# Performance work log

Hardware: AMD Instinct MI355X
Metric: run time of the kernel (lower is better)

## Reference

```python
import jax, jax.numpy as jnp
import numpy as np

EMBED_DIM = 1024
NUM_HEADS = 16
HEAD_DIM = EMBED_DIM // NUM_HEADS
SCALE_BASE = EMBED_DIM  # XPOS(head_dim, embed_dim): embed_dim is scale_base
BSZ, SEQ = 8, 1024


def xpos_apply(x, downscale):
    # x: [B*H, L, D]; standard xpos (torchscale) rotary with position-dependent scale
    L, D = x.shape[1], x.shape[2]
    half = D // 2
    s = (jnp.arange(0, D, 2, dtype=jnp.float32) + 0.4 * D) / (1.4 * D)  # [half]
    min_pos = -(L // 2)  # offset = 0
    pos = jnp.arange(min_pos, min_pos + L, dtype=jnp.float32)  # [L]
    scale = s[None, :] ** (pos[:, None] / SCALE_BASE)  # [L, half]
    inv_freq = 1.0 / (10000.0 ** (jnp.arange(half, dtype=jnp.float32) / half))
    sinus = jnp.arange(L, dtype=jnp.float32)[:, None] * inv_freq[None, :]  # [L, half]
    sin, cos = jnp.sin(sinus), jnp.cos(sinus)
    if downscale:
        scale = 1.0 / scale
    # duplicate_interleave: repeat each column twice -> [L, D]
    sin_d = jnp.repeat(sin * scale, 2, axis=-1)
    cos_d = jnp.repeat(cos * scale, 2, axis=-1)
    x1, x2 = x[..., 0::2], x[..., 1::2]
    rot = jnp.stack([-x2, x1], axis=-1).reshape(x.shape)  # rotate_every_two
    return x * cos_d + rot * sin_d


def setup_inputs() -> dict:
    key = jax.random.key(0)
    ks = jax.random.split(key, 12)
    std = 0.02
    inp = {
        'query': jax.random.normal(ks[0], (BSZ, SEQ, EMBED_DIM), jnp.float32),
        'key': jax.random.normal(ks[1], (BSZ, SEQ, EMBED_DIM), jnp.float32),
        'value': jax.random.normal(ks[2], (BSZ, SEQ, EMBED_DIM), jnp.float32),
        'wq': jax.random.normal(ks[3], (EMBED_DIM, EMBED_DIM), jnp.float32) * std,
        'bq': jax.random.normal(ks[4], (EMBED_DIM,), jnp.float32) * std,
        'wk': jax.random.normal(ks[5], (EMBED_DIM, EMBED_DIM), jnp.float32) * std,
        'bk': jax.random.normal(ks[6], (EMBED_DIM,), jnp.float32) * std,
        'wv': jax.random.normal(ks[7], (EMBED_DIM, EMBED_DIM), jnp.float32) * std,
        'bv': jax.random.normal(ks[8], (EMBED_DIM,), jnp.float32) * std,
        'wo': jax.random.normal(ks[9], (EMBED_DIM, EMBED_DIM), jnp.float32) * std,
        'bo': jax.random.normal(ks[10], (EMBED_DIM,), jnp.float32) * std,
    }
    return inp


def reference(query, key, value, wq, bq, wk, bk, wv, bv, wo, bo):
    B, T, E = query.shape
    S = key.shape[1]
    scaling = HEAD_DIM ** -0.5
    q = (query @ wq.T + bq) * scaling
    k = key @ wk.T + bk
    v = value @ wv.T + bv

    def split_heads(x, L):
        return x.reshape(B, L, NUM_HEADS, HEAD_DIM).transpose(0, 2, 1, 3).reshape(B * NUM_HEADS, L, HEAD_DIM)

    q = split_heads(q, T)
    k = split_heads(k, S)
    v = split_heads(v, S)
    k = xpos_apply(k, downscale=True)
    q = xpos_apply(q, downscale=False)
    attn_w = jnp.einsum('btd,bsd->bts', q, k)  # [B*H, T, S]
    attn_w = jax.nn.softmax(attn_w.astype(jnp.float32), axis=-1).astype(q.dtype)
    attn = jnp.einsum('bts,bsd->btd', attn_w, v)  # [B*H, T, D]
    attn = attn.reshape(B, NUM_HEADS, T, HEAD_DIM).transpose(0, 2, 1, 3).reshape(B, T, E)
    return attn @ wo.T + bo
```

## Files before the change

kernel.cpp:

```cpp
#include <hip/hip_runtime.h>


#define BSZ  8
#define SEQ  1024
#define EMB  1024
#define NH   16
#define HD   64
#define HALF 32
#define BH   (BSZ*NH)
#define MROWS (BSZ*SEQ)

typedef __attribute__((ext_vector_type(4))) float f32x4;
typedef __attribute__((ext_vector_type(8))) short bf16x8;

__device__ __forceinline__ ushort f2bf(float f) {
    union { float f; unsigned u; } v; v.f = f;
    return (ushort)((v.u + 0x7FFFu + ((v.u >> 16) & 1u)) >> 16);
}

__device__ __forceinline__ unsigned cvt_pk_bf16(float a, float b) {
    unsigned r;
    asm("v_cvt_pk_bf16_f32 %0, %1, %2" : "=v"(r) : "v"(a), "v"(b));
    return r;
}

__device__ __forceinline__ void async16(void* lds, const void* g) {
    __builtin_amdgcn_global_load_lds(
        (const __attribute__((address_space(1))) unsigned int*)g,
        (__attribute__((address_space(3))) unsigned int*)lds, 16, 0, 0);
}

__global__ __launch_bounds__(256)
void castw_kernel(const float* __restrict__ w0, const float* __restrict__ w1,
                  const float* __restrict__ w2, const float* __restrict__ w3,
                  ushort* __restrict__ d0, ushort* __restrict__ d1,
                  ushort* __restrict__ d2, ushort* __restrict__ d3, int n4) {
    int i = blockIdx.x * 256 + threadIdx.x;
    if (i >= n4) return;
    const float* s = blockIdx.y == 0 ? w0 : blockIdx.y == 1 ? w1
                   : blockIdx.y == 2 ? w2 : w3;
    ushort* d = blockIdx.y == 0 ? d0 : blockIdx.y == 1 ? d1
              : blockIdx.y == 2 ? d2 : d3;
    float4 v = reinterpret_cast<const float4*>(s)[i];
    ushort4 o;
    o.x = f2bf(v.x); o.y = f2bf(v.y); o.z = f2bf(v.z); o.w = f2bf(v.w);
    reinterpret_cast<ushort4*>(d)[i] = o;
}

__global__ __launch_bounds__(256)
void xpos_tables_kernel(float* __restrict__ tab) {
    int idx = blockIdx.x * 256 + threadIdx.x;
    if (idx >= SEQ * HALF) return;
    int t = idx >> 5;
    int j = idx & 31;
    float s        = (2.0f * (float)j + 0.4f * (float)HD) / (1.4f * (float)HD);
    float pos      = (float)(t - SEQ / 2);
    float scale    = powf(s, pos * (1.0f / 1024.0f));
    float inv_freq = powf(10000.0f, -(float)j / (float)HALF);
    float ang      = (float)t * inv_freq;
    float sn = sinf(ang), cs = cosf(ang);
    float inv_scale = 1.0f / scale;
    tab[0 * SEQ * HALF + idx] = sn * scale;
    tab[1 * SEQ * HALF + idx] = cs * scale;
    tab[2 * SEQ * HALF + idx] = sn * inv_scale;
    tab[3 * SEQ * HALF + idx] = cs * inv_scale;
}

__global__ __launch_bounds__(256, 3)
void qkv_gemm_kernel(const float* __restrict__ Aq, const float* __restrict__ Ak,
                     const float* __restrict__ Av,
                     const ushort* __restrict__ Wq, const ushort* __restrict__ Wk,
                     const ushort* __restrict__ Wv,
                     const float* __restrict__ bq, const float* __restrict__ bk,
                     const float* __restrict__ bv,
                     const float* __restrict__ tab,
                     ushort* __restrict__ oq, ushort* __restrict__ ok,
                     ushort* __restrict__ ov) {
    __shared__ float  Asf[128 * 64];
    __shared__ ushort Bs[128 * 64];
    const int ymode = blockIdx.y;
    const float*  A    = ymode == 0 ? Aq : ymode == 1 ? Ak : Av;
    const ushort* W    = ymode == 0 ? Wq : ymode == 1 ? Wk : Wv;
    const float*  bias = ymode == 0 ? bq : ymode == 1 ? bk : bv;
    ushort*       outp = ymode == 0 ? oq : ymode == 1 ? ok : ov;

    const int tid  = threadIdx.x;
    const int lane = tid & 63;
    const int w    = tid >> 6;
    const int g    = lane >> 4;
    const int c    = lane & 15;
    const int wr   = w >> 1, wc = w & 1;

    int lid = blockIdx.x;
    int wg  = (lid & 7) * 64 + (lid >> 3);
    const int row0 = (wg >> 3) * 128;
    const int col0 = (wg & 7) * 128;

    f32x4 acc[4][4] = {};

    int arow[8], acol[8];
    #pragma unroll
    for (int i = 0; i < 8; ++i) {
        int f = i * 4096 + tid * 16;
        int r = f >> 8, pb = f & 255;
        arow[i] = r;
        acol[i] = (pb ^ ((r & 7) << 5)) >> 2;
    }
    int brow[4], bcol[4];
    #pragma unroll
    for (int i = 0; i < 4; ++i) {
        int f = i * 4096 + tid * 16;
        int r = f >> 7, cb = f & 127;
        brow[i] = r;
        bcol[i] = (cb ^ ((r & 7) << 4)) >> 1;
    }

    for (int t = 0; t < 16; ++t) {
        const int k0 = t * 64;
        #pragma unroll
        for (int i = 0; i < 8; ++i)
            async16(&Asf[i * 1024 + w * 256],
                    &A[(size_t)(row0 + arow[i]) * EMB + k0 + acol[i]]);
        #pragma unroll
        for (int i = 0; i < 4; ++i)
            async16(&Bs[i * 2048 + w * 512],
                    &W[(size_t)(col0 + brow[i]) * EMB + k0 + bcol[i]]);
        __syncthreads();

        #pragma unroll
        for (int ks = 0; ks < 2; ++ks) {
            bf16x8 af[4], bfr[4];
            #pragma unroll
            for (int mi = 0; mi < 4; ++mi) {
                int r  = wr * 64 + mi * 16 + c;
                int pb = (ks * 128 + g * 32) ^ ((r & 7) << 5);
                const char* ab = reinterpret_cast<const char*>(Asf) + r * 256 + pb;
                f32x4 a0 = *reinterpret_cast<const f32x4*>(ab);
                f32x4 a1 = *reinterpret_cast<const f32x4*>(ab + 16);
                union { uint4 u; bf16x8 v; } pk;
                pk.u.x = cvt_pk_bf16(a0[0], a0[1]);
                pk.u.y = cvt_pk_bf16(a0[2], a0[3]);
                pk.u.z = cvt_pk_bf16(a1[0], a1[1]);
                pk.u.w = cvt_pk_bf16(a1[2], a1[3]);
                af[mi] = pk.v;
            }
            #pragma unroll
            for (int ni = 0; ni < 4; ++ni) {
                int r = wc * 64 + ni * 16 + c;
                bfr[ni] = *reinterpret_cast<const bf16x8*>(
                    reinterpret_cast<const char*>(Bs) + r * 128 +
                    ((ks * 64 + g * 16) ^ ((r & 7) << 4)));
            }
            #pragma unroll
            for (int mi = 0; mi < 4; ++mi)
                #pragma unroll
                for (int ni = 0; ni < 4; ++ni)
                    acc[mi][ni] = __builtin_amdgcn_mfma_f32_16x16x32_bf16(
                        af[mi], bfr[ni], acc[mi][ni], 0, 0, 0);
        }
        __syncthreads();
    }

    #pragma unroll
    for (int ni = 0; ni < 4; ++ni) {
        int n = col0 + wc * 64 + ni * 16 + c;
        float bn = bias[n];
        #pragma unroll
        for (int mi = 0; mi < 4; ++mi) {
            #pragma unroll
            for (int r = 0; r < 4; ++r) {
                int m = row0 + wr * 64 + mi * 16 + g * 4 + r;
                float val = acc[mi][ni][r] + bn;
                if (ymode == 0) val *= 0.125f;
                if (ymode != 2) {
                    int t2 = m & (SEQ - 1);
                    int d  = n & 63;
                    const int base = (ymode == 0 ? 0 : 2) * SEQ * HALF + t2 * HALF;
                    float sn = tab[base + (d >> 1)];
                    float cs = tab[base + SEQ * HALF + (d >> 1)];
                    float other = __shfl_xor(val, 1);
                    val = val * cs + ((d & 1) ? other * sn : -other * sn);
                }
                int b = m >> 10, t3 = m & 1023;
                int h = n >> 6,  d2 = n & 63;
                outp[(((size_t)b * NH + h) * SEQ + t3) * HD + d2] = f2bf(val);
            }
        }
    }
}

template <int MODE>
__global__ __launch_bounds__(256)
void gemm_bf16_kernel(const ushort* __restrict__ A, const ushort* __restrict__ W,
                      const float* __restrict__ bias, const float* __restrict__ tab,
                      void* __restrict__ outp) {
    __shared__ ushort As[2][128 * 64];
    __shared__ ushort Bs[2][128 * 64];
    const int tid  = threadIdx.x;
    const int lane = tid & 63;
    const int w    = tid >> 6;
    const int g    = lane >> 4;
    const int c    = lane & 15;
    const int wr   = w >> 1, wc = w & 1;

    int lid = blockIdx.x;
    int wg  = (lid & 7) * 64 + (lid >> 3);
    const int row0 = (wg >> 3) * 128;
    const int col0 = (wg & 7) * 128;

    f32x4 acc[4][4] = {};

    int srow[4], scol[4];
    #pragma unroll
    for (int i = 0; i < 4; ++i) {
        int f = i * 4096 + tid * 16;
        int r = f >> 7, cb = f & 127;
        srow[i] = r;
        scol[i] = (cb ^ ((r & 7) << 4)) >> 1;
    }

    auto stage = [&](int buf, int k0) {
        #pragma unroll
        for (int i = 0; i < 4; ++i) {
            const ushort* srcA;
            if (MODE == 3) {
                int h = k0 >> 6;
                srcA = &A[(((size_t)(row0 >> 10) * NH + h) * SEQ +
                           (row0 & 1023) + srow[i]) * HD + scol[i]];
            } else {
                srcA = &A[(size_t)(row0 + srow[i]) * EMB + k0 + scol[i]];
            }
            async16(&As[buf][i * 2048 + w * 512], srcA);
        }
        #pragma unroll
        for (int i = 0; i < 4; ++i)
            async16(&Bs[buf][i * 2048 + w * 512],
                    &W[(size_t)(col0 + srow[i]) * EMB + k0 + scol[i]]);
    };

    stage(0, 0);
    __syncthreads();

    for (int t = 0; t < 16; ++t) {
        const int cur = t & 1;
        if (t < 15) stage(cur ^ 1, (t + 1) * 64);

        const char* abase = reinterpret_cast<const char*>(&As[cur][0]);
        const char* bbase = reinterpret_cast<const char*>(&Bs[cur][0]);
        #pragma unroll
        for (int ks = 0; ks < 2; ++ks) {
            bf16x8 af[4], bfr[4];
            #pragma unroll
            for (int mi = 0; mi < 4; ++mi) {
                int r = wr * 64 + mi * 16 + c;
                af[mi] = *reinterpret_cast<const bf16x8*>(
                    abase + r * 128 + ((ks * 64 + g * 16) ^ ((r & 7) << 4)));
            }
            #pragma unroll
            for (int ni = 0; ni < 4; ++ni) {
                int r = wc * 64 + ni * 16 + c;
                bfr[ni] = *reinterpret_cast<const bf16x8*>(
                    bbase + r * 128 + ((ks * 64 + g * 16) ^ ((r & 7) << 4)));
            }
            #pragma unroll
            for (int mi = 0; mi < 4; ++mi)
                #pragma unroll
                for (int ni = 0; ni < 4; ++ni)
                    acc[mi][ni] = __builtin_amdgcn_mfma_f32_16x16x32_bf16(
                        af[mi], bfr[ni], acc[mi][ni], 0, 0, 0);
        }
        __syncthreads();
    }

    #pragma unroll
    for (int ni = 0; ni < 4; ++ni) {
        int n = col0 + wc * 64 + ni * 16 + c;
        float bn = bias[n];
        #pragma unroll
        for (int mi = 0; mi < 4; ++mi) {
            #pragma unroll
            for (int r = 0; r < 4; ++r) {
                int m = row0 + wr * 64 + mi * 16 + g * 4 + r;
                float val = acc[mi][ni][r] + bn;
                if (MODE == 3) {
                    ((float*)outp)[(size_t)m * EMB + n] = val;
                } else {
                    int b = m >> 10, t2 = m & 1023;
                    int h = n >> 6,  d = n & 63;
                    ((ushort*)outp)[(((size_t)b * NH + h) * SEQ + t2) * HD + d] =
                        f2bf(val);
                }
            }
        }
    }
}

__global__ __launch_bounds__(256)
void vtrans_kernel(const ushort* __restrict__ v, ushort* __restrict__ vt) {
    __shared__ ushort T[64][72];
    const int tid = threadIdx.x;
    const int bh  = blockIdx.y;
    const int t0  = blockIdx.x * 64;
    const ushort* vb = &v[((size_t)bh * SEQ + t0) * HD];
    #pragma unroll
    for (int p = 0; p < 2; ++p) {
        int chunk = p * 256 + tid;
        int tl = chunk >> 3;
        int d8 = (chunk & 7) * 8;
        ushort tmp[8];
        *reinterpret_cast<uint4*>(tmp) =
            *reinterpret_cast<const uint4*>(&vb[tl * HD + d8]);
        #pragma unroll
        for (int j = 0; j < 8; ++j) T[d8 + j][tl] = tmp[j];
    }
    __syncthreads();
    ushort* ob = &vt[(size_t)bh * HD * SEQ + t0];
    #pragma unroll
    for (int p = 0; p < 2; ++p) {
        int chunk = p * 256 + tid;
        int dl = chunk >> 3;
        int t8 = (chunk & 7) * 8;
        *reinterpret_cast<uint4*>(&ob[(size_t)dl * SEQ + t8]) =
            *reinterpret_cast<const uint4*>(&T[dl][t8]);
    }
}

__global__ __launch_bounds__(512, 6)
void attn_kernel(const ushort* __restrict__ qg, const ushort* __restrict__ kg,
                 const ushort* __restrict__ vtg, ushort* __restrict__ og) {
    __shared__ ushort Ks[2 * 4096];
    __shared__ ushort Vs[2 * 4096];
    __shared__ ushort Ps[8 * 1024];
    const int tid  = threadIdx.x;
    const int lane = tid & 63;
    const int w    = tid >> 6;
    const int g    = lane >> 4;
    const int c    = lane & 15;

    int lid = blockIdx.x;
    int wg  = (lid & 7) * 128 + (lid >> 3);
    const int bh = wg >> 3;
    const int q0 = (wg & 7) * 128;

    const ushort* qrow = &qg[((size_t)bh * SEQ + q0 + w * 16 + c) * HD];
    bf16x8 qf[2];
    qf[0] = *reinterpret_cast<const bf16x8*>(qrow + g * 8);
    qf[1] = *reinterpret_cast<const bf16x8*>(qrow + 32 + g * 8);

    float m_run[4], l_part[4];
    f32x4 oacc[4] = {};
    #pragma unroll
    for (int r = 0; r < 4; ++r) { m_run[r] = -1e30f; l_part[r] = 0.f; }

    const int sf   = tid * 16;
    const int srow = sf >> 7;
    const int scol = ((sf & 127) ^ ((srow & 7) << 4)) >> 1;

    const ushort* kb  = &kg[(size_t)bh * SEQ * HD];
    const ushort* vtb = &vtg[(size_t)bh * HD * SEQ];

    auto stage = [&](int buf, int kt) {
        async16(&Ks[buf * 4096 + w * 512],
                &kb[(size_t)(kt + srow) * HD + scol]);
        async16(&Vs[buf * 4096 + w * 512],
                &vtb[(size_t)srow * SEQ + kt + scol]);
    };

    stage(0, 0);
    __syncthreads();

    char* pbase = reinterpret_cast<char*>(Ps) + w * 2048;

    for (int kt = 0; kt < SEQ; kt += 64) {
        const int cur = (kt >> 6) & 1;
        if (kt + 64 < SEQ) stage(cur ^ 1, kt + 64);

        const char* kbase = reinterpret_cast<const char*>(Ks) + cur * 8192;
        const char* vbase = reinterpret_cast<const char*>(Vs) + cur * 8192;

        f32x4 s[4];
        #pragma unroll
        for (int j = 0; j < 4; ++j) {
            int key = j * 16 + c;
            int sw  = (key & 7) << 4;
            f32x4 a = {};
            #pragma unroll
            for (int ks = 0; ks < 2; ++ks) {
                bf16x8 kf = *reinterpret_cast<const bf16x8*>(
                    kbase + key * 128 + ((ks * 64 + g * 16) ^ sw));
                a = __builtin_amdgcn_mfma_f32_16x16x32_bf16(qf[ks], kf, a, 0, 0, 0);
            }
            s[j] = a;
        }

        float pmax[4];
        #pragma unroll
        for (int r = 0; r < 4; ++r)
            pmax[r] = fmaxf(fmaxf(s[0][r], s[1][r]), fmaxf(s[2][r], s[3][r]));
        int need = (pmax[0] > m_run[0] + 8.f) || (pmax[1] > m_run[1] + 8.f) ||
                   (pmax[2] > m_run[2] + 8.f) || (pmax[3] > m_run[3] + 8.f);
        if (__any(need)) {
            #pragma unroll
            for (int r = 0; r < 4; ++r) {
                float mx = pmax[r];
                mx = fmaxf(mx, __shfl_xor(mx, 1));
                mx = fmaxf(mx, __shfl_xor(mx, 2));
                mx = fmaxf(mx, __shfl_xor(mx, 4));
                mx = fmaxf(mx, __shfl_xor(mx, 8));
                float mn = fmaxf(m_run[r], mx);
                float alpha = __expf(m_run[r] - mn);
                l_part[r] *= alpha;
                #pragma unroll
                for (int dblk = 0; dblk < 4; ++dblk) oacc[dblk][r] *= alpha;
                m_run[r] = mn;
            }
        }

        #pragma unroll
        for (int r = 0; r < 4; ++r) {
            int q  = g * 4 + r;
            int sw = (q & 7) << 4;
            #pragma unroll
            for (int j = 0; j < 4; ++j) {
                float p = __expf(s[j][r] - m_run[r]);
                l_part[r] += p;
                int byt = q * 128 + (((j * 16 + c) * 2) ^ sw);
                *reinterpret_cast<ushort*>(pbase + byt) = f2bf(p);
            }
        }

        #pragma unroll
        for (int ks = 0; ks < 2; ++ks) {
            bf16x8 pf = *reinterpret_cast<const bf16x8*>(
                pbase + c * 128 + ((ks * 64 + g * 16) ^ ((c & 7) << 4)));
            #pragma unroll
            for (int dblk = 0; dblk < 4; ++dblk) {
                int d = dblk * 16 + c;
                bf16x8 vf = *reinterpret_cast<const bf16x8*>(
                    vbase + d * 128 + ((ks * 64 + g * 16) ^ ((d & 7) << 4)));
                oacc[dblk] = __builtin_amdgcn_mfma_f32_16x16x32_bf16(
                    pf, vf, oacc[dblk], 0, 0, 0);
            }
        }
        __syncthreads();
    }

    #pragma unroll
    for (int r = 0; r < 4; ++r) {
        float rs = l_part[r];
        rs += __shfl_xor(rs, 1);
        rs += __shfl_xor(rs, 2);
        rs += __shfl_xor(rs, 4);
        rs += __shfl_xor(rs, 8);
        float inv = 1.f / rs;
        int q = q0 + w * 16 + g * 4 + r;
        #pragma unroll
        for (int dblk = 0; dblk < 4; ++dblk)
            og[((size_t)bh * SEQ + q) * HD + dblk * 16 + c] =
                f2bf(oacc[dblk][r] * inv);
    }
}

extern "C" void kernel_launch(void* const* d_in, const int* in_sizes, int n_in,
                              void* d_out, int out_size, void* d_ws,
                              size_t ws_size, hipStream_t stream) {
    const float* query = (const float*)d_in[0];
    const float* key_  = (const float*)d_in[1];
    const float* value = (const float*)d_in[2];
    const float* wq    = (const float*)d_in[3];
    const float* bq    = (const float*)d_in[4];
    const float* wk    = (const float*)d_in[5];
    const float* bk    = (const float*)d_in[6];
    const float* wv    = (const float*)d_in[7];
    const float* bv    = (const float*)d_in[8];
    const float* wo    = (const float*)d_in[9];
    const float* bo    = (const float*)d_in[10];

    ushort* ws16 = (ushort*)d_ws;
    const size_t NX = (size_t)MROWS * EMB;
    const size_t NW = (size_t)EMB * EMB;
    ushort* wqb = ws16;
    ushort* wkb = wqb + NW;
    ushort* wvb = wkb + NW;
    ushort* wob = wvb + NW;
    float*  tab = (float*)(wob + NW);
    ushort* qb  = (ushort*)(tab + 4 * SEQ * HALF);
    ushort* kb  = qb + NX;
    ushort* vb  = kb + NX;
    ushort* vt  = vb + NX;
    ushort* ob  = vt + NX;

    const int nw4 = (int)(NW / 4);

    castw_kernel<<<dim3(nw4 / 256, 4), 256, 0, stream>>>(
        wq, wk, wv, wo, wqb, wkb, wvb, wob, nw4);
    xpos_tables_kernel<<<SEQ * HALF / 256, 256, 0, stream>>>(tab);

    qkv_gemm_kernel<<<dim3(512, 3), 256, 0, stream>>>(
        query, key_, value, wqb, wkb, wvb, bq, bk, bv, tab, qb, kb, vb);

    vtrans_kernel<<<dim3(16, 128), 256, 0, stream>>>(vb, vt);

    attn_kernel<<<1024, 512, 0, stream>>>(qb, kb, vt, ob);

    gemm_bf16_kernel<3><<<512, 256, 0, stream>>>(ob, wob, bo, nullptr,
                                                 (float*)d_out);
}
```

Measured before the change: 377.6 us.

## Halve attention query tile to 64 rows and rework fp32 A-tile LDS swizzle

The attention kernel now uses 256-thread blocks over 64 query rows, with 2048 blocks instead of 1024. Each thread issues two async K/V loads per stage instead of one, and the P scratch buffer shrinks to match. Separately, the QKV GEMM's fp32 A-tile swizzle now XORs at 16-byte granularity and computes the two 16-byte reads independently, to cut LDS bank conflicts. Smaller attention blocks give more blocks and finer scheduling, but each block reloads the full K/V stream for fewer queries, so K/V traffic per query doubles.

```diff
diff --git a/kernel.cpp b/kernel.cpp
--- a/kernel.cpp
+++ b/kernel.cpp
@@ -104,7 +104,7 @@
         int f = i * 4096 + tid * 16;
         int r = f >> 8, pb = f & 255;
         arow[i] = r;
-        acol[i] = (pb ^ ((r & 7) << 5)) >> 2;
+        acol[i] = (pb ^ ((r & 7) << 4)) >> 2;
     }
     int brow[4], bcol[4];
     #pragma unroll
@@ -132,11 +132,13 @@
             bf16x8 af[4], bfr[4];
             #pragma unroll
             for (int mi = 0; mi < 4; ++mi) {
-                int r  = wr * 64 + mi * 16 + c;
-                int pb = (ks * 128 + g * 32) ^ ((r & 7) << 5);
-                const char* ab = reinterpret_cast<const char*>(Asf) + r * 256 + pb;
-                f32x4 a0 = *reinterpret_cast<const f32x4*>(ab);
-                f32x4 a1 = *reinterpret_cast<const f32x4*>(ab + 16);
+                int r   = wr * 64 + mi * 16 + c;
+                int sw  = (r & 7) << 4;
+                int pb0 = (ks * 128 + g * 32) ^ sw;
+                int pb1 = pb0 ^ 16;
+                const char* ab = reinterpret_cast<const char*>(Asf) + r * 256;
+                f32x4 a0 = *reinterpret_cast<const f32x4*>(ab + pb0);
+                f32x4 a1 = *reinterpret_cast<const f32x4*>(ab + pb1);
                 union { uint4 u; bf16x8 v; } pk;
                 pk.u.x = cvt_pk_bf16(a0[0], a0[1]);
                 pk.u.y = cvt_pk_bf16(a0[2], a0[3]);
@@ -325,12 +327,12 @@
     }
 }
 
-__global__ __launch_bounds__(512, 6)
+__global__ __launch_bounds__(256)
 void attn_kernel(const ushort* __restrict__ qg, const ushort* __restrict__ kg,
                  const ushort* __restrict__ vtg, ushort* __restrict__ og) {
     __shared__ ushort Ks[2 * 4096];
     __shared__ ushort Vs[2 * 4096];
-    __shared__ ushort Ps[8 * 1024];
+    __shared__ ushort Ps[4096];
     const int tid  = threadIdx.x;
     const int lane = tid & 63;
     const int w    = tid >> 6;
@@ -338,9 +340,9 @@
     const int c    = lane & 15;
 
     int lid = blockIdx.x;
-    int wg  = (lid & 7) * 128 + (lid >> 3);
-    const int bh = wg >> 3;
-    const int q0 = (wg & 7) * 128;
+    int wg  = (lid & 7) * 256 + (lid >> 3);
+    const int bh = wg >> 4;
+    const int q0 = (wg & 15) * 64;
 
     const ushort* qrow = &qg[((size_t)bh * SEQ + q0 + w * 16 + c) * HD];
     bf16x8 qf[2];
@@ -352,18 +354,25 @@
     #pragma unroll
     for (int r = 0; r < 4; ++r) { m_run[r] = -1e30f; l_part[r] = 0.f; }
 
-    const int sf   = tid * 16;
-    const int srow = sf >> 7;
-    const int scol = ((sf & 127) ^ ((srow & 7) << 4)) >> 1;
+    int srow[2], scol[2];
+    #pragma unroll
+    for (int i = 0; i < 2; ++i) {
+        int f = i * 4096 + tid * 16;
+        int r = f >> 7, cb = f & 127;
+        srow[i] = r; scol[i] = (cb ^ ((r & 7) << 4)) >> 1;
+    }
 
     const ushort* kb  = &kg[(size_t)bh * SEQ * HD];
     const ushort* vtb = &vtg[(size_t)bh * HD * SEQ];
 
     auto stage = [&](int buf, int kt) {
-        async16(&Ks[buf * 4096 + w * 512],
-                &kb[(size_t)(kt + srow) * HD + scol]);
-        async16(&Vs[buf * 4096 + w * 512],
-                &vtb[(size_t)srow * SEQ + kt + scol]);
+        #pragma unroll
+        for (int i = 0; i < 2; ++i) {
+            async16(&Ks[buf * 4096 + i * 2048 + w * 512],
+                    &kb[(size_t)(kt + srow[i]) * HD + scol[i]]);
+            async16(&Vs[buf * 4096 + i * 2048 + w * 512],
+                    &vtb[(size_t)srow[i] * SEQ + kt + scol[i]]);
+        }
     };
 
     stage(0, 0);
@@ -501,7 +510,7 @@
 
     vtrans_kernel<<<dim3(16, 128), 256, 0, stream>>>(vb, vt);
 
-    attn_kernel<<<1024, 512, 0, stream>>>(qb, kb, vt, ob);
+    attn_kernel<<<2048, 256, 0, stream>>>(qb, kb, vt, ob);
 
     gemm_bf16_kernel<3><<<512, 256, 0, stream>>>(ob, wob, bo, nullptr,
                                                  (float*)d_out);
```

After: 380.4 us. No clear change (+0.7%).
